# Kernel tuning notes

Hardware: AMD Instinct MI355X
Metric: run time of the kernel (lower is better)

The kernel has to match this reference:

```python
import jax, jax.numpy as jnp
import numpy as np

B, D, HID = 16384, 1024, 4096
HALF = D // 2


def setup_inputs() -> dict:
    key = jax.random.key(0)
    ks = jax.random.split(key, 9)
    sc_in = 1.0 / np.sqrt(HALF)
    sc_h = 1.0 / np.sqrt(HID)
    return {
        "z": jax.random.normal(ks[0], (B, D), dtype=jnp.float32),
        "W1s": jax.random.uniform(ks[1], (HALF, HID), jnp.float32, -sc_in, sc_in),
        "b1s": jax.random.uniform(ks[2], (HID,), jnp.float32, -sc_in, sc_in),
        "W2s": jax.random.uniform(ks[3], (HID, HALF), jnp.float32, -sc_h, sc_h),
        "b2s": jax.random.uniform(ks[4], (HALF,), jnp.float32, -sc_h, sc_h),
        "W1t": jax.random.uniform(ks[5], (HALF, HID), jnp.float32, -sc_in, sc_in),
        "b1t": jax.random.uniform(ks[6], (HID,), jnp.float32, -sc_in, sc_in),
        "W2t": jax.random.uniform(ks[7], (HID, HALF), jnp.float32, -sc_h, sc_h),
        "b2t": jax.random.uniform(ks[8], (HALF,), jnp.float32, -sc_h, sc_h),
    }


def reference(z, W1s, b1s, W2s, b2s, W1t, b1t, W2t, b2t):
    # mask_even=True: a = even-indexed features, b = odd-indexed features
    a = z[:, 0::2]  # [B, HALF]
    b = z[:, 1::2]  # [B, HALF]
    # two-layer MLPs for s and t (cond=None -> inp = a)
    s = jnp.maximum(a @ W1s + b1s, 0.0) @ W2s + b2s  # [B, HALF]
    t = jnp.maximum(a @ W1t + b1t, 0.0) @ W2t + b2t  # [B, HALF]
    b_out = b * jnp.exp(s) + t
    logdet = s.sum(axis=1)  # [B]
    # scatter back: a -> even slots, b_out -> odd slots (interleave)
    z_out = jnp.stack([a, b_out], axis=-1).reshape(z.shape)
    return z_out, logdet
```

## Files before the change

kernel.cpp:

```cpp
#include <hip/hip_runtime.h>
#include <hip/hip_bf16.h>
#include <cstdint>
#include <cstddef>

#define BROWS  16384
#define DDIM   1024
#define HID_N  4096
#define HALF_K 512
#define LDH    8192

typedef __attribute__((ext_vector_type(8))) short s8v;
typedef __attribute__((ext_vector_type(4))) float f4v;
typedef __attribute__((ext_vector_type(2))) float f2v;

__device__ __forceinline__ void gload16(const void* g, void* l) {
  __builtin_amdgcn_global_load_lds(
      (const __attribute__((address_space(1))) unsigned int*)g,
      (__attribute__((address_space(3))) unsigned int*)l, 16, 0, 0);
}
#define BAR()   asm volatile("s_barrier" ::: "memory")
#define BARS()  asm volatile("s_waitcnt lgkmcnt(0)\n\ts_barrier" ::: "memory")
#define SCHED0() __builtin_amdgcn_sched_barrier(0)

template <int N> __device__ __forceinline__ void vmw() {
  if constexpr (N == 0)      asm volatile("s_waitcnt vmcnt(0)" ::: "memory");
  else if constexpr (N == 4) asm volatile("s_waitcnt vmcnt(4)" ::: "memory");
  else if constexpr (N == 8) asm volatile("s_waitcnt vmcnt(8)" ::: "memory");
}

__device__ __forceinline__ void transpose_body(const float* __restrict__ W,
                                               __hip_bfloat16* __restrict__ WT,
                                               int K, int N, int bx, int by) {
  __shared__ float tile[32][33];
  const int n0 = bx * 32, k0 = by * 32;
  const int tx = threadIdx.x & 31;
  const int ty = threadIdx.x >> 5;
#pragma unroll
  for (int i = 0; i < 32; i += 8)
    tile[ty + i][tx] = W[(size_t)(k0 + ty + i) * N + n0 + tx];
  __syncthreads();
#pragma unroll
  for (int i = 0; i < 32; i += 8)
    WT[(size_t)(n0 + ty + i) * K + k0 + tx] = __float2bfloat16(tile[tx][ty + i]);
}

__global__ __launch_bounds__(256) void prep_kernel(const float* __restrict__ z,
                                                   __hip_bfloat16* __restrict__ a16,
                                                   const float* __restrict__ W1s,
                                                   const float* __restrict__ W1t,
                                                   const float* __restrict__ W2s,
                                                   const float* __restrict__ W2t,
                                                   __hip_bfloat16* __restrict__ w1T,
                                                   __hip_bfloat16* __restrict__ w2sT,
                                                   __hip_bfloat16* __restrict__ w2tT) {
  const int b = blockIdx.x;
  if (b < 4096) {
    const int idx = b * 256 + threadIdx.x;
    const int m  = idx >> 6;
    const int kb = idx & 63;
    const float4* zp = (const float4*)(z + (size_t)m * DDIM + (size_t)kb * 16);
    alignas(16) __hip_bfloat16 t[8];
#pragma unroll
    for (int i = 0; i < 4; ++i) {
      float4 v = zp[i];
      t[2 * i]     = __float2bfloat16(v.x);
      t[2 * i + 1] = __float2bfloat16(v.z);
    }
    *(s8v*)(a16 + (size_t)m * HALF_K + kb * 8) = *(const s8v*)t;
  } else if (b < 6144) {
    const int v = b - 4096;
    transpose_body(W1s, w1T, HALF_K, HID_N, v & 127, v >> 7);
  } else if (b < 8192) {
    const int v = b - 6144;
    transpose_body(W1t, w1T + (size_t)HID_N * HALF_K, HALF_K, HID_N, v & 127, v >> 7);
  } else if (b < 10240) {
    const int v = b - 8192;
    transpose_body(W2s, w2sT, HID_N, HALF_K, v & 15, v >> 4);
  } else {
    const int v = b - 10240;
    transpose_body(W2t, w2tT, HID_N, HALF_K, v & 15, v >> 4);
  }
}

__global__ __launch_bounds__(512, 2)
void gemm1_kernel(const __hip_bfloat16* __restrict__ A,
                  const __hip_bfloat16* __restrict__ BT,
                  const float* __restrict__ b1s, const float* __restrict__ b1t,
                  __hip_bfloat16* __restrict__ Hout) {
  __shared__ alignas(16) char smem[131072];
  constexpr int NT = HALF_K / 64;

  const int nwg = gridDim.x;
  const int orig = blockIdx.x;
  const int vid = (orig & 7) * (nwg >> 3) + (orig >> 3);
  const int bx = vid >> 5, by = vid & 31;
  const int m0 = bx * 256, n0 = by * 256;

  const int tid = threadIdx.x;
  const int trow = tid >> 3;
  const int scol = ((tid & 7) * 16) ^ ((trow & 7) << 4);

  const int lane = tid & 63, wid = tid >> 6;
  const int wr = wid >> 2, wc = wid & 3;
  const int lr = lane & 15, lk = lane >> 4;
  const int xo = (lr & 7) << 4;

  int aoff[4][2], boff[2][2];
#pragma unroll
  for (int j = 0; j < 4; ++j)
#pragma unroll
    for (int kk = 0; kk < 2; ++kk)
      aoff[j][kk] = (j * 32 + wr * 16 + lr) * 128 + ((kk * 64 + lk * 16) ^ xo);
#pragma unroll
  for (int nn = 0; nn < 2; ++nn)
#pragma unroll
    for (int kk = 0; kk < 2; ++kk)
      boff[nn][kk] = (nn * 64 + wc * 16 + lr) * 128 + ((kk * 64 + lk * 16) ^ xo);

  f4v acc[8][4] = {};

  auto stage_A = [&](int h, int T) {
#pragma unroll
    for (int l = 0; l < 2; ++l)
      gload16((const char*)A + (size_t)(m0 + h * 128 + l * 64 + trow) * (HALF_K * 2) + (size_t)T * 128 + scol,
              smem + (T & 1) * 65536 + h * 16384 + l * 8192 + tid * 16);
  };
  auto stage_B = [&](int h, int T) {
#pragma unroll
    for (int l = 0; l < 2; ++l)
      gload16((const char*)BT + (size_t)(n0 + h * 128 + l * 64 + trow) * (HALF_K * 2) + (size_t)T * 128 + scol,
              smem + (T & 1) * 65536 + 32768 + h * 16384 + l * 8192 + tid * 16);
  };

  stage_A(0, 0); stage_B(0, 0); stage_A(1, 0); stage_B(1, 0);
  stage_A(0, 1); stage_B(0, 1);
  vmw<4>();
  BAR();

  for (int T = 0; T < NT; ++T) {
    const char* bufp = smem + (T & 1) * 65536;
    s8v af[4][2], b0r[2][2], b1r[2][2];

#pragma unroll
    for (int j = 0; j < 4; ++j) {
      af[j][0] = *(const s8v*)(bufp + aoff[j][0]);
      af[j][1] = *(const s8v*)(bufp + aoff[j][1]);
    }
#pragma unroll
    for (int nn = 0; nn < 2; ++nn) {
      b0r[nn][0] = *(const s8v*)(bufp + 32768 + boff[nn][0]);
      b0r[nn][1] = *(const s8v*)(bufp + 32768 + boff[nn][1]);
    }
    if (T + 1 < NT) stage_B(1, T + 1);
    BAR(); SCHED0();
    __builtin_amdgcn_s_setprio(1);
#pragma unroll
    for (int j = 0; j < 4; ++j)
#pragma unroll
      for (int nn = 0; nn < 2; ++nn)
#pragma unroll
        for (int kk = 0; kk < 2; ++kk)
          acc[j][nn] = __builtin_amdgcn_mfma_f32_16x16x32_bf16(af[j][kk], b0r[nn][kk], acc[j][nn], 0, 0, 0);
    __builtin_amdgcn_s_setprio(0);
    BAR();

#pragma unroll
    for (int nn = 0; nn < 2; ++nn) {
      b1r[nn][0] = *(const s8v*)(bufp + 49152 + boff[nn][0]);
      b1r[nn][1] = *(const s8v*)(bufp + 49152 + boff[nn][1]);
    }
    if (T + 1 < NT) stage_A(1, T + 1);
    BAR(); SCHED0();
    __builtin_amdgcn_s_setprio(1);
#pragma unroll
    for (int j = 0; j < 4; ++j)
#pragma unroll
      for (int nn = 0; nn < 2; ++nn)
#pragma unroll
        for (int kk = 0; kk < 2; ++kk)
          acc[j][2 + nn] = __builtin_amdgcn_mfma_f32_16x16x32_bf16(af[j][kk], b1r[nn][kk], acc[j][2 + nn], 0, 0, 0);
    __builtin_amdgcn_s_setprio(0);
    BAR();

#pragma unroll
    for (int j = 0; j < 4; ++j) {
      af[j][0] = *(const s8v*)(bufp + 16384 + aoff[j][0]);
      af[j][1] = *(const s8v*)(bufp + 16384 + aoff[j][1]);
    }
    if (T + 2 < NT) stage_A(0, T + 2);
    BAR(); SCHED0();
    __builtin_amdgcn_s_setprio(1);
#pragma unroll
    for (int j = 0; j < 4; ++j)
#pragma unroll
      for (int nn = 0; nn < 2; ++nn)
#pragma unroll
        for (int kk = 0; kk < 2; ++kk)
          acc[4 + j][nn] = __builtin_amdgcn_mfma_f32_16x16x32_bf16(af[j][kk], b0r[nn][kk], acc[4 + j][nn], 0, 0, 0);
    __builtin_amdgcn_s_setprio(0);
    BAR();

    if (T + 2 < NT) stage_B(0, T + 2);
    SCHED0();
    __builtin_amdgcn_s_setprio(1);
#pragma unroll
    for (int j = 0; j < 4; ++j)
#pragma unroll
      for (int nn = 0; nn < 2; ++nn)
#pragma unroll
        for (int kk = 0; kk < 2; ++kk)
          acc[4 + j][2 + nn] = __builtin_amdgcn_mfma_f32_16x16x32_bf16(af[j][kk], b1r[nn][kk], acc[4 + j][2 + nn], 0, 0, 0);
    __builtin_amdgcn_s_setprio(0);
    if (T + 2 >= NT) vmw<0>(); else vmw<4>();
    BAR();
  }

  const float* bp = (n0 < HID_N) ? b1s : b1t;
  const int cb0 = n0 & (HID_N - 1);
  float bv[4];
#pragma unroll
  for (int ni = 0; ni < 4; ++ni) bv[ni] = bp[cb0 + ni * 64 + wc * 16 + lr];

#pragma unroll
  for (int mi = 0; mi < 8; ++mi) {
#pragma unroll
    for (int ni = 0; ni < 4; ++ni) {
      const int cb = (ni * 64 + wc * 16 + lr) * 2;
#pragma unroll
      for (int r = 0; r < 4; ++r) {
        const int row = mi * 32 + wr * 16 + lk * 4 + r;
        const int swz = ((row & 7) << 4) ^ (((row >> 3) & 1) << 8);
        float v = fmaxf(acc[mi][ni][r] + bv[ni], 0.0f);
        *(__hip_bfloat16*)(smem + row * 512 + (cb ^ swz)) = __float2bfloat16(v);
      }
    }
  }
  BARS();
#pragma unroll
  for (int i = 0; i < 16; ++i) {
    const int bo = tid * 16 + i * 8192;
    const int row = bo >> 9, cb = bo & 511;
    const int swz = ((row & 7) << 4) ^ (((row >> 3) & 1) << 8);
    s8v v = *(const s8v*)(smem + row * 512 + (cb ^ swz));
    *(s8v*)((char*)Hout + ((size_t)(m0 + row) * LDH + n0) * 2 + cb) = v;
  }
}

__global__ __launch_bounds__(512, 2)
void gemm2_kernel(const __hip_bfloat16* __restrict__ H,
                  const __hip_bfloat16* __restrict__ BsT,
                  const __hip_bfloat16* __restrict__ BtT,
                  const float* __restrict__ b2s, const float* __restrict__ b2t,
                  const float* __restrict__ zin, float* __restrict__ zout,
                  float* __restrict__ gpart) {
  __shared__ alignas(16) char smem[131072];
  constexpr int NT = HID_N / 32;

  const int nwg = gridDim.x;
  const int orig = blockIdx.x;
  const int vid = (orig & 7) * (nwg >> 3) + (orig >> 3);
  const int rb = vid >> 2, by = vid & 3;
  const int m0 = rb * 128, n0c = by * 128;

  const int tid = threadIdx.x;
  const int trow = tid >> 2;
  const int scol = (((tid & 3) ^ ((tid >> 3) & 3)) << 4);

  const int lane = tid & 63, wid = tid >> 6;
  const int ws = wid & 1, wc = (wid >> 1) & 1, wr = (wid >> 2) & 1;
  const int lr = lane & 15, lk = lane >> 4;
  const int xo2 = ((lr >> 1) & 3) << 4;

  const int aBase = ws ? 8192 : 0;
  const int bBase = ws ? 24576 : 16384;
  int aoff[4], boff[4];
#pragma unroll
  for (int f = 0; f < 4; ++f) {
    aoff[f] = aBase + (wr * 64 + f * 16 + lr) * 64 + ((lk * 16) ^ xo2);
    boff[f] = bBase + (wc * 64 + f * 16 + lr) * 64 + ((lk * 16) ^ xo2);
  }

  f4v acc[4][4] = {};

  auto stage = [&](int T) {
    char* dst = smem + (T & 3) * 32768;
    const size_t tcol = (size_t)T * 64 + scol;
    gload16((const char*)H + (size_t)(m0 + trow) * (LDH * 2) + tcol, dst + tid * 16);
    gload16((const char*)H + (size_t)(m0 + trow) * (LDH * 2) + 8192 + tcol, dst + 8192 + tid * 16);
    gload16((const char*)BsT + (size_t)(n0c + trow) * (HID_N * 2) + tcol, dst + 16384 + tid * 16);
    gload16((const char*)BtT + (size_t)(n0c + trow) * (HID_N * 2) + tcol, dst + 24576 + tid * 16);
  };

  stage(0); stage(1); stage(2);
  vmw<8>();
  BAR();

  for (int T = 0; T < NT; ++T) {
    const char* bufp = smem + (T & 3) * 32768;
    s8v af[4], bf[4];
#pragma unroll
    for (int f = 0; f < 4; ++f) af[f] = *(const s8v*)(bufp + aoff[f]);
#pragma unroll
    for (int f = 0; f < 4; ++f) bf[f] = *(const s8v*)(bufp + boff[f]);
    if (T + 3 < NT) stage(T + 3);
    __builtin_amdgcn_s_setprio(1);
#pragma unroll
    for (int fm = 0; fm < 4; ++fm)
#pragma unroll
      for (int fn = 0; fn < 4; ++fn)
        acc[fm][fn] = __builtin_amdgcn_mfma_f32_16x16x32_bf16(af[fm], bf[fn], acc[fm][fn], 0, 0, 0);
    __builtin_amdgcn_s_setprio(0);
    if (T + 3 < NT)      vmw<8>();
    else if (T + 2 < NT) vmw<4>();
    else if (T + 1 < NT) vmw<0>();
    BAR();
  }

  const float* bp2 = ws ? b2t : b2s;
  float bv[4];
#pragma unroll
  for (int fn = 0; fn < 4; ++fn) bv[fn] = bp2[n0c + wc * 64 + fn * 16 + lr];

  float* slds = (float*)smem;
  if (ws == 0) {
#pragma unroll
    for (int fm = 0; fm < 4; ++fm)
#pragma unroll
      for (int fn = 0; fn < 4; ++fn)
#pragma unroll
        for (int r = 0; r < 4; ++r) {
          const int row = wr * 64 + fm * 16 + lk * 4 + r;
          const int col = wc * 64 + fn * 16 + lr;
          slds[row * 132 + col] = acc[fm][fn][r] + bv[fn];
        }
  }
  BARS();
  if (ws == 1) {
    float pl[4][4] = {};
#pragma unroll
    for (int fm = 0; fm < 4; ++fm) {
#pragma unroll
      for (int fn = 0; fn < 4; ++fn) {
#pragma unroll
        for (int r = 0; r < 4; ++r) {
          const int row = wr * 64 + fm * 16 + lk * 4 + r;
          const int col = wc * 64 + fn * 16 + lr;
          const int rr = m0 + row;
          const float sv = slds[row * 132 + col];
          const float tv = acc[fm][fn][r] + bv[fn];
          pl[fm][r] += sv;
          const size_t base = (size_t)rr * DDIM + 2 * (size_t)(n0c + col);
          float2 zv = *(const float2*)(zin + base);
          f2v o;
          o.x = zv.x;
          o.y = zv.y * __expf(sv) + tv;
          __builtin_nontemporal_store(o, (f2v*)(zout + base));
        }
      }
    }
#pragma unroll
    for (int m = 1; m < 16; m <<= 1)
#pragma unroll
      for (int fm = 0; fm < 4; ++fm)
#pragma unroll
        for (int r = 0; r < 4; ++r)
          pl[fm][r] += __shfl_xor(pl[fm][r], m, 64);
    if (lr == 0) {
#pragma unroll
      for (int fm = 0; fm < 4; ++fm)
#pragma unroll
        for (int r = 0; r < 4; ++r) {
          const int rr = m0 + wr * 64 + fm * 16 + lk * 4 + r;
          gpart[(size_t)rr * 8 + by * 2 + wc] = pl[fm][r];
        }
    }
  }
}

__global__ __launch_bounds__(256) void ld_reduce_kernel(const float* __restrict__ gpart,
                                                        float* __restrict__ ld) {
  const int r = blockIdx.x * 256 + threadIdx.x;
  const float4* g = (const float4*)(gpart + (size_t)r * 8);
  float4 v0 = g[0], v1 = g[1];
  ld[r] = ((v0.x + v0.y) + (v0.z + v0.w)) + ((v1.x + v1.y) + (v1.z + v1.w));
}

extern "C" void kernel_launch(void* const* d_in, const int* in_sizes, int n_in,
                              void* d_out, int out_size, void* d_ws, size_t ws_size,
                              hipStream_t stream) {
  const float* z   = (const float*)d_in[0];
  const float* W1s = (const float*)d_in[1];
  const float* b1s = (const float*)d_in[2];
  const float* W2s = (const float*)d_in[3];
  const float* b2s = (const float*)d_in[4];
  const float* W1t = (const float*)d_in[5];
  const float* b1t = (const float*)d_in[6];
  const float* W2t = (const float*)d_in[7];
  const float* b2t = (const float*)d_in[8];
  float* zout = (float*)d_out;
  float* ld   = zout + (size_t)BROWS * DDIM;

  char* ws = (char*)d_ws;
  __hip_bfloat16* a16    = (__hip_bfloat16*)ws;
  __hip_bfloat16* w1catT = (__hip_bfloat16*)(ws + 16777216);
  __hip_bfloat16* w2sT   = (__hip_bfloat16*)(ws + 25165824);
  __hip_bfloat16* w2tT   = (__hip_bfloat16*)(ws + 29360128);
  float*          gpart  = (float*)(ws + 33554432);
  char*           hbase  = ws + 34078720;

  int CH = 2048;
  for (int c = 8192; c >= 2048; c >>= 1) {
    if (34078720ull + (size_t)c * 16384ull <= ws_size) { CH = c; break; }
  }
  __hip_bfloat16* H = (__hip_bfloat16*)hbase;

  prep_kernel<<<12288, 256, 0, stream>>>(z, a16, W1s, W1t, W2s, W2t,
                                         w1catT, w2sT, w2tT);

  const int SUB = (CH >= 4096) ? 4096 : CH;
  for (int mb = 0; mb < BROWS; mb += CH) {
    for (int sub = 0; sub < CH; sub += SUB) {
      gemm1_kernel<<<(SUB / 256) * 32, 512, 0, stream>>>(
          a16 + (size_t)(mb + sub) * HALF_K, w1catT, b1s, b1t,
          H + (size_t)sub * LDH);
    }
    gemm2_kernel<<<(CH / 128) * 4, 512, 0, stream>>>(
        H, w2sT, w2tT, b2s, b2t,
        z + (size_t)mb * DDIM, zout + (size_t)mb * DDIM, gpart + (size_t)mb * 8);
  }
  ld_reduce_kernel<<<BROWS / 256, 256, 0, stream>>>(gpart, ld);
}
```

Before: 392.4 us.

## Shrink gemm2 tile to 128x64 with 256 threads and double-buffered LDS

Measured after the change: 421.8 us. 1.07x slower.

```diff
diff --git a/kernel.cpp b/kernel.cpp
--- a/kernel.cpp
+++ b/kernel.cpp
@@ -246,63 +246,70 @@
   }
 }
 
-__global__ __launch_bounds__(512, 2)
+__global__ __launch_bounds__(256, 2)
 void gemm2_kernel(const __hip_bfloat16* __restrict__ H,
                   const __hip_bfloat16* __restrict__ BsT,
                   const __hip_bfloat16* __restrict__ BtT,
                   const float* __restrict__ b2s, const float* __restrict__ b2t,
                   const float* __restrict__ zin, float* __restrict__ zout,
                   float* __restrict__ gpart) {
-  __shared__ alignas(16) char smem[131072];
+  __shared__ alignas(16) char smem[49152];
   constexpr int NT = HID_N / 32;
 
   const int nwg = gridDim.x;
   const int orig = blockIdx.x;
   const int vid = (orig & 7) * (nwg >> 3) + (orig >> 3);
-  const int rb = vid >> 2, by = vid & 3;
-  const int m0 = rb * 128, n0c = by * 128;
+  const int rb = vid >> 3, by = vid & 7;
+  const int m0 = rb * 128, n0c = by * 64;
 
   const int tid = threadIdx.x;
   const int trow = tid >> 2;
   const int scol = (((tid & 3) ^ ((tid >> 3) & 3)) << 4);
 
   const int lane = tid & 63, wid = tid >> 6;
-  const int ws = wid & 1, wc = (wid >> 1) & 1, wr = (wid >> 2) & 1;
+  const int ws = wid & 1, wm = wid >> 1;
   const int lr = lane & 15, lk = lane >> 4;
   const int xo2 = ((lr >> 1) & 3) << 4;
 
   const int aBase = ws ? 8192 : 0;
-  const int bBase = ws ? 24576 : 16384;
+  const int bBase = ws ? 20480 : 16384;
   int aoff[4], boff[4];
 #pragma unroll
   for (int f = 0; f < 4; ++f) {
-    aoff[f] = aBase + (wr * 64 + f * 16 + lr) * 64 + ((lk * 16) ^ xo2);
-    boff[f] = bBase + (wc * 64 + f * 16 + lr) * 64 + ((lk * 16) ^ xo2);
+    aoff[f] = aBase + (wm * 64 + f * 16 + lr) * 64 + ((lk * 16) ^ xo2);
+    boff[f] = bBase + (f * 16 + lr) * 64 + ((lk * 16) ^ xo2);
   }
 
   f4v acc[4][4] = {};
 
   auto stage = [&](int T) {
-    char* dst = smem + (T & 3) * 32768;
+    char* dst = smem + (T & 1) * 24576;
     const size_t tcol = (size_t)T * 64 + scol;
-    gload16((const char*)H + (size_t)(m0 + trow) * (LDH * 2) + tcol, dst + tid * 16);
-    gload16((const char*)H + (size_t)(m0 + trow) * (LDH * 2) + 8192 + tcol, dst + 8192 + tid * 16);
-    gload16((const char*)BsT + (size_t)(n0c + trow) * (HID_N * 2) + tcol, dst + 16384 + tid * 16);
-    gload16((const char*)BtT + (size_t)(n0c + trow) * (HID_N * 2) + tcol, dst + 24576 + tid * 16);
+#pragma unroll
+    for (int l = 0; l < 2; ++l) {
+      gload16((const char*)H + (size_t)(m0 + l * 64 + trow) * (LDH * 2) + tcol,
+              dst + l * 4096 + tid * 16);
+      gload16((const char*)H + (size_t)(m0 + l * 64 + trow) * (LDH * 2) + 8192 + tcol,
+              dst + 8192 + l * 4096 + tid * 16);
+    }
+    gload16((const char*)BsT + (size_t)(n0c + trow) * (HID_N * 2) + tcol,
+            dst + 16384 + tid * 16);
+    gload16((const char*)BtT + (size_t)(n0c + trow) * (HID_N * 2) + tcol,
+            dst + 20480 + tid * 16);
   };
 
-  stage(0); stage(1); stage(2);
-  vmw<8>();
+  stage(0);
+  vmw<0>();
   BAR();
 
   for (int T = 0; T < NT; ++T) {
-    const char* bufp = smem + (T & 3) * 32768;
+    const char* bufp = smem + (T & 1) * 24576;
     s8v af[4], bf[4];
 #pragma unroll
     for (int f = 0; f < 4; ++f) af[f] = *(const s8v*)(bufp + aoff[f]);
 #pragma unroll
     for (int f = 0; f < 4; ++f) bf[f] = *(const s8v*)(bufp + boff[f]);
-    if (T + 3 < NT) stage(T + 3);
+    if (T + 1 < NT) stage(T + 1);
     __builtin_amdgcn_s_setprio(1);
 #pragma unroll
     for (int fm = 0; fm < 4; ++fm)
@@ -310,16 +317,14 @@
       for (int fn = 0; fn < 4; ++fn)
         acc[fm][fn] = __builtin_amdgcn_mfma_f32_16x16x32_bf16(af[fm], bf[fn], acc[fm][fn], 0, 0, 0);
     __builtin_amdgcn_s_setprio(0);
-    if (T + 3 < NT)      vmw<8>();
-    else if (T + 2 < NT) vmw<4>();
-    else if (T + 1 < NT) vmw<0>();
+    if (T + 1 < NT) vmw<0>();
     BAR();
   }
 
   const float* bp2 = ws ? b2t : b2s;
   float bv[4];
 #pragma unroll
-  for (int fn = 0; fn < 4; ++fn) bv[fn] = bp2[n0c + wc * 64 + fn * 16 + lr];
+  for (int fn = 0; fn < 4; ++fn) bv[fn] = bp2[n0c + fn * 16 + lr];
 
   float* slds = (float*)smem;
   if (ws == 0) {
@@ -329,9 +334,8 @@
       for (int fn = 0; fn < 4; ++fn)
 #pragma unroll
         for (int r = 0; r < 4; ++r) {
-          const int row = wr * 64 + fm * 16 + lk * 4 + r;
-          const int col = wc * 64 + fn * 16 + lr;
-          slds[row * 132 + col] = acc[fm][fn][r] + bv[fn];
+          const int row = wm * 64 + fm * 16 + lk * 4 + r;
+          slds[row * 68 + fn * 16 + lr] = acc[fm][fn][r] + bv[fn];
         }
   }
   BARS();
@@ -343,13 +347,13 @@
       for (int fn = 0; fn < 4; ++fn) {
 #pragma unroll
         for (int r = 0; r < 4; ++r) {
-          const int row = wr * 64 + fm * 16 + lk * 4 + r;
-          const int col = wc * 64 + fn * 16 + lr;
+          const int row = wm * 64 + fm * 16 + lk * 4 + r;
           const int rr = m0 + row;
-          const float sv = slds[row * 132 + col];
+          const int cg = n0c + fn * 16 + lr;
+          const float sv = slds[row * 68 + fn * 16 + lr];
           const float tv = acc[fm][fn][r] + bv[fn];
           pl[fm][r] += sv;
-          const size_t base = (size_t)rr * DDIM + 2 * (size_t)(n0c + col);
+          const size_t base = (size_t)rr * DDIM + 2 * (size_t)cg;
           float2 zv = *(const float2*)(zin + base);
           f2v o;
           o.x = zv.x;
@@ -370,8 +374,8 @@
       for (int fm = 0; fm < 4; ++fm)
 #pragma unroll
         for (int r = 0; r < 4; ++r) {
-          const int rr = m0 + wr * 64 + fm * 16 + lk * 4 + r;
-          gpart[(size_t)rr * 8 + by * 2 + wc] = pl[fm][r];
+          const int rr = m0 + wm * 64 + fm * 16 + lk * 4 + r;
+          gpart[(size_t)rr * 8 + by] = pl[fm][r];
         }
     }
   }
@@ -424,7 +428,7 @@
           a16 + (size_t)(mb + sub) * HALF_K, w1catT, b1s, b1t,
           H + (size_t)sub * LDH);
     }
-    gemm2_kernel<<<(CH / 128) * 4, 512, 0, stream>>>(
+    gemm2_kernel<<<(CH / 128) * 8, 256, 0, stream>>>(
         H, w2sT, w2tT, b2s, b2t,
         z + (size_t)mb * DDIM, zout + (size_t)mb * DDIM, gpart + (size_t)mb * 8);
   }
```
